# Performance work log

Measured on AMD Instinct MI355X. Metric: run time of the kernel, lower is better.

## Reference

```python
import jax, jax.numpy as jnp
import numpy as np

N, E, F, EF, H = 10000, 320000, 512, 6, 256


def _lin(k, fan_in, fan_out):
    # torch.nn.Linear default init
    s = 1.0 / np.sqrt(fan_in)
    kw, kb = jax.random.split(k)
    W = jax.random.uniform(kw, (fan_in, fan_out), minval=-s, maxval=s, dtype=jnp.float32)
    b = jax.random.uniform(kb, (fan_out,), minval=-s, maxval=s, dtype=jnp.float32)
    return W, b


def setup_inputs() -> dict:
    key = jax.random.key(0)
    ks = jax.random.split(key, 13)
    inp = {}
    inp["x"] = jax.random.normal(ks[0], (N, F), dtype=jnp.float32)
    inp["edge_index"] = jax.random.randint(ks[1], (2, E), 0, N, dtype=jnp.int32)
    inp["edge_attr"] = jax.random.normal(ks[2], (E, EF), dtype=jnp.float32)
    shapes = {
        "We0a": (2 * F + EF, H), "We0b": (H, H),   # conv_in edge MLP
        "Wn0a": (F + H, H),      "Wn0b": (H, H),   # conv_in node MLP
        "We1a": (3 * H, H),      "We1b": (H, H),   # conv[0] edge MLP
        "Wn1a": (2 * H, H),      "Wn1b": (H, H),   # conv[0] node MLP
        "Wp1":  (H, H),          "Wp2":  (H, 1),   # EdgePredictorFromEdges
    }
    for i, (nm, (fi, fo)) in enumerate(shapes.items()):
        W, b = _lin(ks[3 + i % 10], fi, fo)
        inp[nm] = W
        inp["b" + nm[1:]] = b
    return inp


def _mp(x, src, dst, ea, Wea, bea, Web, beb, Wna, bna, Wnb, bnb, residual, agg_mean):
    # MetaLayer edge model: MLP(concat[x_i, x_j, edge_attr])
    e_in = jnp.concatenate([x[src], x[dst], ea], axis=-1)   # [E, ...]
    new_ea = jax.nn.relu(e_in @ Wea + bea) @ Web + beb
    if residual:
        new_ea = new_ea + ea
    # node model: aggregate incoming edges at dst, MLP(concat[x, agg])
    agg = jax.ops.segment_sum(new_ea, dst, num_segments=N)  # [N, H]
    if agg_mean:
        deg = jax.ops.segment_sum(jnp.ones((src.shape[0],), x.dtype), dst, num_segments=N)
        agg = agg / jnp.maximum(deg, 1.0)[:, None]
    n_in = jnp.concatenate([x, agg], axis=-1)
    new_x = jax.nn.relu(n_in @ Wna + bna) @ Wnb + bnb
    if residual:
        new_x = new_x + x
    return new_x, new_ea


def reference(x, edge_index, edge_attr,
              We0a, be0a, We0b, be0b, Wn0a, bn0a, Wn0b, bn0b,
              We1a, be1a, We1b, be1b, Wn1a, bn1a, Wn1b, bn1b,
              Wp1, bp1, Wp2, bp2):
    src, dst = edge_index[0], edge_index[1]
    # conv_in: dims change (F->H, EF->H) so no residual; base_aggregation='mean'
    x1, ea1 = _mp(x, src, dst, edge_attr, We0a, be0a, We0b, be0b,
                  Wn0a, bn0a, Wn0b, bn0b, residual=False, agg_mean=True)
    # conv[0]: dims match -> residual; default base_aggregation='sum'
    x2, ea2 = _mp(x1, src, dst, ea1, We1a, be1a, We1b, be1b,
                  Wn1a, bn1a, Wn1b, bn1b, residual=True, agg_mean=False)
    # EdgePredictorFromEdges (eval mode -> dropout is identity)
    h = jax.nn.leaky_relu(ea2 @ Wp1 + bp1)
    out = (h @ Wp2 + bp2)[:, 0]  # squeeze -> [E]
    return out
```

## Files before the change

### kernel.cpp

```cpp
#include <hip/hip_runtime.h>

#define N_NODES 10000
#define N_EDGES 320000
#define HD      256

typedef __attribute__((ext_vector_type(8))) short bf16x8;
typedef __attribute__((ext_vector_type(4))) float f32x4;
#define MFMA16 __builtin_amdgcn_mfma_f32_16x16x32_bf16

#define OFF_PD   2560000
#define OFF_BA   5120000
#define OFF_BB   7680000
#define OFF_BC   10240000
#define OFF_DEG  12800000
#define OFF_BCV  12810000
#define OFF_BAV  12810256
#define OFF_PW0  12810512

__device__ __forceinline__ ushort f2bf(float x) {
  union { float f; unsigned u; } c; c.f = x;
  unsigned r = (c.u + 0x7FFFu + ((c.u >> 16) & 1u)) >> 16;
  return (ushort)r;
}
__device__ __forceinline__ float bf2f(ushort h) {
  union { float f; unsigned u; } c; c.u = ((unsigned)h) << 16; return c.f;
}

__global__ __launch_bounds__(256)
void prep_split(const float* __restrict__ W, ushort* __restrict__ H,
                ushort* __restrict__ L)
{
  int slot = blockIdx.x * 256 + threadIdx.x;
  int s    = slot >> 10;
  int rem  = slot & 1023;
  int cf   = rem >> 6;
  int lane = rem & 63;
  int k0 = s * 32 + ((lane >> 4) << 3);
  int n  = cf * 16 + (lane & 15);
#pragma unroll
  for (int j = 0; j < 8; ++j) {
    float v = W[(k0 + j) * HD + n];
    ushort hi = f2bf(v);
    H[slot * 8 + j] = hi;
    L[slot * 8 + j] = f2bf(v - bf2f(hi));
  }
}

__global__ __launch_bounds__(256)
void node_gemm(const float* __restrict__ A1, int K1,
               const float* __restrict__ A2, int K2,
               const float* __restrict__ scale,
               const float* __restrict__ W,
               const float* __restrict__ bias,
               float* __restrict__ C, int M, int act)
{
  __shared__ float sA[64 * 36];
  __shared__ float sB[32 * 256];
  __shared__ float sBias[256];
  const int tid = threadIdx.x;
  const int r0  = blockIdx.x * 64;
  if (bias) sBias[tid] = bias[tid];
  const int ty = tid >> 4, tx = tid & 15;

  float acc[4][16];
#pragma unroll
  for (int r = 0; r < 4; r++)
#pragma unroll
    for (int c = 0; c < 16; c++) acc[r][c] = 0.f;

  const int K = K1 + K2;
  const int arow = tid >> 2;
  const int aks  = (tid & 3) * 8;
  const int gr_a = r0 + arow;

  for (int kb = 0; kb < K; kb += 32) {
    const float* Ap; int lda, koff; float sc = 1.0f;
    if (kb < K1) { Ap = A1; lda = K1; koff = kb; }
    else { Ap = A2; lda = K2; koff = kb - K1;
           if (scale) sc = scale[gr_a < M ? gr_a : M - 1]; }
#pragma unroll
    for (int j = 0; j < 8; j += 4) {
      float4 v;
      if (gr_a < M) v = *(const float4*)&Ap[(long)gr_a * lda + koff + aks + j];
      else { v.x = v.y = v.z = v.w = 0.f; }
      v.x *= sc; v.y *= sc; v.z *= sc; v.w *= sc;
      *(float4*)&sA[arow * 36 + aks + j] = v;
    }
#pragma unroll
    for (int j = 0; j < 8; j++) {
      int i = tid + 256 * j, row = i >> 6, c4 = i & 63;
      *(float4*)&sB[row * HD + c4 * 4] = *(const float4*)&W[(long)(kb + row) * HD + c4 * 4];
    }
    __syncthreads();
#pragma unroll 4
    for (int kk = 0; kk < 32; kk++) {
      float a0 = sA[(ty * 4 + 0) * 36 + kk];
      float a1 = sA[(ty * 4 + 1) * 36 + kk];
      float a2 = sA[(ty * 4 + 2) * 36 + kk];
      float a3 = sA[(ty * 4 + 3) * 36 + kk];
#pragma unroll
      for (int c = 0; c < 16; c++) {
        float b = sB[kk * HD + tx + 16 * c];
        acc[0][c] += a0 * b; acc[1][c] += a1 * b;
        acc[2][c] += a2 * b; acc[3][c] += a3 * b;
      }
    }
    __syncthreads();
  }

#pragma unroll
  for (int r = 0; r < 4; r++) {
    int gr = r0 + ty * 4 + r;
    if (gr >= M) continue;
#pragma unroll
    for (int c = 0; c < 16; c++) {
      int col = tx + 16 * c;
      float v = acc[r][c];
      if (bias) v += sBias[col];
      if (act)  v = fmaxf(v, 0.f);
      C[(long)gr * HD + col] = v;
    }
  }
}

__global__ __launch_bounds__(256)
void bias_fold_k(const float* __restrict__ v1, const float* __restrict__ v2,
                 const float* __restrict__ W, const float* __restrict__ base,
                 float* __restrict__ out)
{
  const int j = threadIdx.x;
  float s = base[j];
  for (int k = 0; k < HD; k++) {
    float v = v1[k] + (v2 ? v2[k] : 0.f);
    s += v * W[k * HD + j];
  }
  out[j] = s;
}

__global__ void rdeg_k(float* __restrict__ deg)
{
  int i = blockIdx.x * blockDim.x + threadIdx.x;
  if (i < N_NODES) deg[i] = 1.0f / fmaxf(deg[i], 1.0f);
}

__device__ __forceinline__ void build_h0(
    int tid, const float* __restrict__ Ps, const float* __restrict__ Pd,
    const float* __restrict__ eattr, long e0,
    const float* __restrict__ W6, const float* __restrict__ b0,
    const int* sSrc, const int* sDst, ushort* Ah, ushort* Al)
{
  const int el = tid >> 3, q = tid & 7;
  const int sv = sSrc[el], dv = sDst[el];
  const long e = e0 + el;
  float eav[6];
#pragma unroll
  for (int k = 0; k < 6; ++k) eav[k] = eattr[e * 6 + k];
  const float* ps = Ps + (long)sv * HD + q * 32;
  const float* pd = Pd + (long)dv * HD + q * 32;
  const int sw = (el & 7) << 4;
  char* ahB = (char*)Ah + el * 512;
  char* alB = (char*)Al + el * 512;
#pragma unroll
  for (int jj = 0; jj < 8; ++jj) {
    float4 a  = *(const float4*)(ps + jj * 4);
    float4 b  = *(const float4*)(pd + jj * 4);
    float4 bb = *(const float4*)(b0 + q * 32 + jj * 4);
    float vx = a.x + b.x + bb.x;
    float vy = a.y + b.y + bb.y;
    float vz = a.z + b.z + bb.z;
    float vw = a.w + b.w + bb.w;
#pragma unroll
    for (int k = 0; k < 6; ++k) {
      float4 w = *(const float4*)(W6 + k * HD + q * 32 + jj * 4);
      vx += eav[k] * w.x; vy += eav[k] * w.y;
      vz += eav[k] * w.z; vw += eav[k] * w.w;
    }
    vx = fmaxf(vx, 0.f); vy = fmaxf(vy, 0.f);
    vz = fmaxf(vz, 0.f); vw = fmaxf(vw, 0.f);
    ushort4 hh, ll;
    hh.x = f2bf(vx); hh.y = f2bf(vy); hh.z = f2bf(vz); hh.w = f2bf(vw);
    ll.x = f2bf(vx - bf2f(hh.x)); ll.y = f2bf(vy - bf2f(hh.y));
    ll.z = f2bf(vz - bf2f(hh.z)); ll.w = f2bf(vw - bf2f(hh.w));
    const int off = (q * 64 + jj * 8) ^ sw;
    *(ushort4*)(ahB + off) = hh;
    *(ushort4*)(alB + off) = ll;
  }
}

__device__ __forceinline__ void write_split(ushort* Ah, ushort* Al,
                                            int row, int col, float v)
{
  const int off = row * 512 + ((col * 2) ^ ((row & 7) << 4));
  ushort hi = f2bf(v);
  *(ushort*)((char*)Ah + off) = hi;
  *(ushort*)((char*)Al + off) = f2bf(v - bf2f(hi));
}

__device__ __forceinline__ void load_afrag(const ushort* Ah, const ushort* Al,
    int row, int s, int lane, bf16x8& ah, bf16x8& al)
{
  const int aoff = row * 512 + ((((s << 6) + ((lane >> 4) << 4))) ^ ((row & 7) << 4));
  ah = *(const bf16x8*)((const char*)Ah + aoff);
  al = *(const bf16x8*)((const char*)Al + aoff);
}

__device__ __forceinline__ void gemm_pass(
    const ushort* __restrict__ pW,
    const ushort* Ah, const ushort* Al,
    int lane, int wc, int wrg, f32x4 acc[2][4])
{
  const bf16x8* pH = (const bf16x8*)pW;
  const bf16x8* pL = (const bf16x8*)(pW + 65536);
#pragma unroll 2
  for (int s = 0; s < 8; ++s) {
    bf16x8 ah[2], al[2];
#pragma unroll
    for (int rb = 0; rb < 2; ++rb)
      load_afrag(Ah, Al, (wrg * 2 + rb) * 16 + (lane & 15), s, lane, ah[rb], al[rb]);
#pragma unroll
    for (int cf = 0; cf < 4; ++cf) {
      const int slot = s * 1024 + (wc * 4 + cf) * 64 + lane;
      bf16x8 bh = pH[slot];
      bf16x8 bl = pL[slot];
#pragma unroll
      for (int rb = 0; rb < 2; ++rb) {
        acc[rb][cf] = MFMA16(al[rb], bh, acc[rb][cf], 0, 0, 0);
        acc[rb][cf] = MFMA16(ah[rb], bl, acc[rb][cf], 0, 0, 0);
        acc[rb][cf] = MFMA16(ah[rb], bh, acc[rb][cf], 0, 0, 0);
      }
    }
  }
}

__global__ __launch_bounds__(512, 4)
void edge_conv_in(const int* __restrict__ ei, const float* __restrict__ eattr,
                  const float* __restrict__ Ps, const float* __restrict__ Pd,
                  const float* __restrict__ W6, const float* __restrict__ b0,
                  const ushort* __restrict__ pW0,
                  const float* __restrict__ be0b,
                  float* __restrict__ agg, float* __restrict__ deg)
{
  __shared__ ushort Ah[64 * 256];
  __shared__ ushort Al[64 * 256];
  __shared__ int    sSrc[64], sDst[64];
  const int tid = threadIdx.x;
  const long e0 = (long)blockIdx.x * 64;

  if (tid < 64) {
    int dv = ei[N_EDGES + e0 + tid];
    sDst[tid] = dv;
    atomicAdd(&deg[dv], 1.0f);
  } else if (tid < 128) {
    sSrc[tid - 64] = ei[e0 + tid - 64];
  }
  __syncthreads();

  build_h0(tid, Ps, Pd, eattr, e0, W6, b0, sSrc, sDst, Ah, Al);
  __syncthreads();

  const int lane = tid & 63, wid = tid >> 6;
  const int wc = wid & 3, wrg = wid >> 2;

  f32x4 acc[2][4];
#pragma unroll
  for (int rb = 0; rb < 2; ++rb)
#pragma unroll
    for (int cf = 0; cf < 4; ++cf) acc[rb][cf] = (f32x4){0.f, 0.f, 0.f, 0.f};
  gemm_pass(pW0, Ah, Al, lane, wc, wrg, acc);

#pragma unroll
  for (int rb = 0; rb < 2; ++rb) {
    const int rbase = (wrg * 2 + rb) * 16 + ((lane >> 4) << 2);
#pragma unroll
    for (int cf = 0; cf < 4; ++cf) {
      const int col = wc * 64 + cf * 16 + (lane & 15);
      const float bv = be0b[col];
#pragma unroll
      for (int r = 0; r < 4; ++r)
        atomicAdd(&agg[(long)sDst[rbase + r] * HD + col], acc[rb][cf][r] + bv);
    }
  }
}

__global__ __launch_bounds__(512, 4)
void edge_pred(const int* __restrict__ ei, const float* __restrict__ eattr,
               const float* __restrict__ Ps, const float* __restrict__ Pd,
               const float* __restrict__ W6, const float* __restrict__ b0,
               const float* __restrict__ P1s, const float* __restrict__ P1d,
               const ushort* __restrict__ pWA, const ushort* __restrict__ pWB,
               const ushort* __restrict__ pWc,
               const float* __restrict__ bA, const float* __restrict__ bc,
               const float* __restrict__ Wp2, const float* __restrict__ bp2,
               float* __restrict__ out)
{
  __shared__ ushort Ah[64 * 256];
  __shared__ ushort Al[64 * 256];
  __shared__ float  sOut[64];
  __shared__ int    sSrc[64], sDst[64];
  const int tid = threadIdx.x;
  const long e0 = (long)blockIdx.x * 64;

  if (tid < 64) {
    sDst[tid] = ei[N_EDGES + e0 + tid];
    sOut[tid] = bp2[0];
  } else if (tid < 128) {
    sSrc[tid - 64] = ei[e0 + tid - 64];
  }
  __syncthreads();

  build_h0(tid, Ps, Pd, eattr, e0, W6, b0, sSrc, sDst, Ah, Al);
  __syncthreads();

  const int lane = tid & 63, wid = tid >> 6;
  const int wc = wid & 3, wrg = wid >> 2;

  f32x4 acc1[2][4];
#pragma unroll
  for (int rb = 0; rb < 2; ++rb)
#pragma unroll
    for (int cf = 0; cf < 4; ++cf) acc1[rb][cf] = (f32x4){0.f, 0.f, 0.f, 0.f};
  gemm_pass(pWA, Ah, Al, lane, wc, wrg, acc1);

  f32x4 accT[2][4];
#pragma unroll
  for (int rb = 0; rb < 2; ++rb)
#pragma unroll
    for (int cf = 0; cf < 4; ++cf) accT[rb][cf] = (f32x4){0.f, 0.f, 0.f, 0.f};
  gemm_pass(pWB, Ah, Al, lane, wc, wrg, accT);
  __syncthreads();

#pragma unroll
  for (int rb = 0; rb < 2; ++rb) {
    const int rbase = (wrg * 2 + rb) * 16 + ((lane >> 4) << 2);
#pragma unroll
    for (int cf = 0; cf < 4; ++cf) {
      const int col = wc * 64 + cf * 16 + (lane & 15);
      const float bv = bA[col];
#pragma unroll
      for (int r = 0; r < 4; ++r) {
        const int row = rbase + r;
        float v = acc1[rb][cf][r] + P1s[(long)sSrc[row] * HD + col]
                                  + P1d[(long)sDst[row] * HD + col] + bv;
        write_split(Ah, Al, row, col, fmaxf(v, 0.f));
      }
    }
  }
  __syncthreads();

  f32x4 accZ[2][4];
#pragma unroll
  for (int rb = 0; rb < 2; ++rb)
#pragma unroll
    for (int cf = 0; cf < 4; ++cf) accZ[rb][cf] = (f32x4){0.f, 0.f, 0.f, 0.f};
  gemm_pass(pWc, Ah, Al, lane, wc, wrg, accZ);

  float p[2][4] = {{0.f,0.f,0.f,0.f},{0.f,0.f,0.f,0.f}};
#pragma unroll
  for (int cf = 0; cf < 4; ++cf) {
    const int col = wc * 64 + cf * 16 + (lane & 15);
    const float w   = Wp2[col];
    const float bcv = bc[col];
#pragma unroll
    for (int rb = 0; rb < 2; ++rb)
#pragma unroll
      for (int r = 0; r < 4; ++r) {
        float z = accZ[rb][cf][r] + accT[rb][cf][r] + bcv;
        z = z > 0.f ? z : 0.01f * z;
        p[rb][r] += z * w;
      }
  }
#pragma unroll
  for (int rb = 0; rb < 2; ++rb)
#pragma unroll
    for (int r = 0; r < 4; ++r) {
      p[rb][r] += __shfl_xor(p[rb][r], 1);
      p[rb][r] += __shfl_xor(p[rb][r], 2);
      p[rb][r] += __shfl_xor(p[rb][r], 4);
      p[rb][r] += __shfl_xor(p[rb][r], 8);
    }
  if ((lane & 15) == 0) {
#pragma unroll
    for (int rb = 0; rb < 2; ++rb) {
      const int rbase = (wrg * 2 + rb) * 16 + ((lane >> 4) << 2);
#pragma unroll
      for (int r = 0; r < 4; ++r) atomicAdd(&sOut[rbase + r], p[rb][r]);
    }
  }
  __syncthreads();
  if (tid < 64) out[e0 + tid] = sOut[tid];
}

extern "C" void kernel_launch(void* const* d_in, const int* in_sizes, int n_in,
                              void* d_out, int out_size, void* d_ws, size_t ws_size,
                              hipStream_t stream)
{
  const float* x     = (const float*)d_in[0];
  const int*   ei    = (const int*)d_in[1];
  const float* eattr = (const float*)d_in[2];
  const float* We0a  = (const float*)d_in[3];
  const float* be0a  = (const float*)d_in[4];
  const float* We0b  = (const float*)d_in[5];
  const float* be0b  = (const float*)d_in[6];
  const float* Wn0a  = (const float*)d_in[7];
  const float* bn0a  = (const float*)d_in[8];
  const float* Wn0b  = (const float*)d_in[9];
  const float* bn0b  = (const float*)d_in[10];
  const float* We1a  = (const float*)d_in[11];
  const float* be1a  = (const float*)d_in[12];
  const float* We1b  = (const float*)d_in[13];
  const float* be1b  = (const float*)d_in[14];
  const float* Wp1   = (const float*)d_in[19];
  const float* bp1   = (const float*)d_in[20];
  const float* Wp2   = (const float*)d_in[21];
  const float* bp2   = (const float*)d_in[22];
  float* out = (float*)d_out;
  float* ws  = (float*)d_ws;

  float* P_s  = ws;
  float* P_d  = ws + OFF_PD;
  float* bufA = ws + OFF_BA;
  float* bufB = ws + OFF_BB;
  float* bufC = ws + OFF_BC;
  float* deg  = ws + OFF_DEG;
  float* bcB  = ws + OFF_BCV;
  float* bAB  = ws + OFF_BAV;
  ushort* pW0 = (ushort*)(ws + OFF_PW0);

  float*  WAf = ws + OFF_BB;
  float*  WBf = ws + OFF_BB + 65536;
  float*  WcF = ws + OFF_BB + 131072;
  ushort* pWA = (ushort*)(ws + OFF_BB + 196608);
  ushort* pWB = (ushort*)(ws + OFF_BB + 262144);
  ushort* pWc = (ushort*)(ws + OFF_BB + 327680);

  const float* W6  = We0a + 1024 * HD;
  const float* WeE = We1a + 512 * HD;

  hipMemsetAsync(bufC, 0, (2560000 + 10000) * sizeof(float), stream);

  const int ngrid = (N_NODES + 63) / 64;
  const int egrid = N_EDGES / 64;

  node_gemm<<<ngrid, 256, 0, stream>>>(x, 512, nullptr, 0, nullptr, We0a,            nullptr, P_s, N_NODES, 0);
  node_gemm<<<ngrid, 256, 0, stream>>>(x, 512, nullptr, 0, nullptr, We0a + 512 * HD, nullptr, P_d, N_NODES, 0);
  prep_split<<<32, 256, 0, stream>>>(We0b, pW0, pW0 + 65536);
  bias_fold_k<<<1, 256, 0, stream>>>(be1b, be0b, Wp1, bp1, bcB);
  bias_fold_k<<<1, 256, 0, stream>>>(be0b, nullptr, WeE, be1a, bAB);

  edge_conv_in<<<egrid, 512, 0, stream>>>(ei, eattr, P_s, P_d, W6, be0a,
                                          pW0, be0b, bufC, deg);
  rdeg_k<<<(N_NODES + 255) / 256, 256, 0, stream>>>(deg);

  node_gemm<<<ngrid, 256, 0, stream>>>(x, 512, bufC, 256, deg, Wn0a, bn0a, bufA, N_NODES, 1);
  node_gemm<<<ngrid, 256, 0, stream>>>(bufA, 256, nullptr, 0, nullptr, Wn0b, bn0b, bufB, N_NODES, 0);
  node_gemm<<<ngrid, 256, 0, stream>>>(bufB, 256, nullptr, 0, nullptr, We1a,            nullptr, bufA, N_NODES, 0);
  node_gemm<<<ngrid, 256, 0, stream>>>(bufB, 256, nullptr, 0, nullptr, We1a + 256 * HD, nullptr, bufC, N_NODES, 0);

  node_gemm<<<4, 256, 0, stream>>>(We0b, 256, nullptr, 0, nullptr, WeE, nullptr, WAf, 256, 0);
  node_gemm<<<4, 256, 0, stream>>>(We0b, 256, nullptr, 0, nullptr, Wp1, nullptr, WBf, 256, 0);
  node_gemm<<<4, 256, 0, stream>>>(We1b, 256, nullptr, 0, nullptr, Wp1, nullptr, WcF, 256, 0);
  prep_split<<<32, 256, 0, stream>>>(WAf, pWA, pWA + 65536);
  prep_split<<<32, 256, 0, stream>>>(WBf, pWB, pWB + 65536);
  prep_split<<<32, 256, 0, stream>>>(WcF, pWc, pWc + 65536);

  edge_pred<<<egrid, 512, 0, stream>>>(ei, eattr, P_s, P_d, W6, be0a,
      bufA, bufC, pWA, pWB, pWc, bAB, bcB, Wp2, bp2, out);
}
```

Baseline: 2.453 ms.

## Retile edge GEMM waves to full-row column strips with B-fragment prefetch

Changes the per-wave MFMA tile from 32 rows x 64 columns to 64 rows x 32 columns, so each wave loads half as many weight fragments from global memory but reads all A fragments from LDS. Adds register double-buffering that prefetches the next k-step's weight fragments while the current step's MFMAs run, and fully unrolls the k loop. This aims to cut global/L2 weight traffic and hide its latency, at the cost of more LDS reads and higher register pressure under the existing launch bounds.

```diff
diff --git a/kernel.cpp b/kernel.cpp
--- a/kernel.cpp
+++ b/kernel.cpp
@@ -207,27 +207,43 @@
 __device__ __forceinline__ void gemm_pass(
     const ushort* __restrict__ pW,
     const ushort* Ah, const ushort* Al,
-    int lane, int wc, int wrg, f32x4 acc[2][4])
+    int lane, int wid, f32x4 acc[4][2])
 {
   const bf16x8* pH = (const bf16x8*)pW;
   const bf16x8* pL = (const bf16x8*)(pW + 65536);
-#pragma unroll 2
+  const int cbase = wid * 2 * 64 + lane;
+  bf16x8 bh[2], bl[2];
+#pragma unroll
+  for (int cf = 0; cf < 2; ++cf) {
+    bh[cf] = pH[cbase + cf * 64];
+    bl[cf] = pL[cbase + cf * 64];
+  }
+#pragma unroll
   for (int s = 0; s < 8; ++s) {
-    bf16x8 ah[2], al[2];
-#pragma unroll
-    for (int rb = 0; rb < 2; ++rb)
-      load_afrag(Ah, Al, (wrg * 2 + rb) * 16 + (lane & 15), s, lane, ah[rb], al[rb]);
-#pragma unroll
-    for (int cf = 0; cf < 4; ++cf) {
-      const int slot = s * 1024 + (wc * 4 + cf) * 64 + lane;
-      bf16x8 bh = pH[slot];
-      bf16x8 bl = pL[slot];
-#pragma unroll
-      for (int rb = 0; rb < 2; ++rb) {
-        acc[rb][cf] = MFMA16(al[rb], bh, acc[rb][cf], 0, 0, 0);
-        acc[rb][cf] = MFMA16(ah[rb], bl, acc[rb][cf], 0, 0, 0);
-        acc[rb][cf] = MFMA16(ah[rb], bh, acc[rb][cf], 0, 0, 0);
+    bf16x8 nbh[2], nbl[2];
+    if (s < 7) {
+      const int slotn = (s + 1) * 1024 + cbase;
+#pragma unroll
+      for (int cf = 0; cf < 2; ++cf) {
+        nbh[cf] = pH[slotn + cf * 64];
+        nbl[cf] = pL[slotn + cf * 64];
       }
+    }
+    bf16x8 ah[4], al[4];
+#pragma unroll
+    for (int rb = 0; rb < 4; ++rb)
+      load_afrag(Ah, Al, rb * 16 + (lane & 15), s, lane, ah[rb], al[rb]);
+#pragma unroll
+    for (int cf = 0; cf < 2; ++cf)
+#pragma unroll
+      for (int rb = 0; rb < 4; ++rb) {
+        acc[rb][cf] = MFMA16(al[rb], bh[cf], acc[rb][cf], 0, 0, 0);
+        acc[rb][cf] = MFMA16(ah[rb], bl[cf], acc[rb][cf], 0, 0, 0);
+        acc[rb][cf] = MFMA16(ah[rb], bh[cf], acc[rb][cf], 0, 0, 0);
+      }
+    if (s < 7) {
+#pragma unroll
+      for (int cf = 0; cf < 2; ++cf) { bh[cf] = nbh[cf]; bl[cf] = nbl[cf]; }
     }
   }
 }
@@ -259,21 +275,20 @@
   __syncthreads();
 
   const int lane = tid & 63, wid = tid >> 6;
-  const int wc = wid & 3, wrg = wid >> 2;
-
-  f32x4 acc[2][4];
-#pragma unroll
-  for (int rb = 0; rb < 2; ++rb)
-#pragma unroll
-    for (int cf = 0; cf < 4; ++cf) acc[rb][cf] = (f32x4){0.f, 0.f, 0.f, 0.f};
-  gemm_pass(pW0, Ah, Al, lane, wc, wrg, acc);
-
-#pragma unroll
-  for (int rb = 0; rb < 2; ++rb) {
-    const int rbase = (wrg * 2 + rb) * 16 + ((lane >> 4) << 2);
-#pragma unroll
-    for (int cf = 0; cf < 4; ++cf) {
-      const int col = wc * 64 + cf * 16 + (lane & 15);
+
+  f32x4 acc[4][2];
+#pragma unroll
+  for (int rb = 0; rb < 4; ++rb)
+#pragma unroll
+    for (int cf = 0; cf < 2; ++cf) acc[rb][cf] = (f32x4){0.f, 0.f, 0.f, 0.f};
+  gemm_pass(pW0, Ah, Al, lane, wid, acc);
+
+#pragma unroll
+  for (int rb = 0; rb < 4; ++rb) {
+    const int rbase = rb * 16 + ((lane >> 4) << 2);
+#pragma unroll
+    for (int cf = 0; cf < 2; ++cf) {
+      const int col = wid * 32 + cf * 16 + (lane & 15);
       const float bv = be0b[col];
 #pragma unroll
       for (int r = 0; r < 4; ++r)
@@ -312,29 +327,28 @@
   __syncthreads();
 
   const int lane = tid & 63, wid = tid >> 6;
-  const int wc = wid & 3, wrg = wid >> 2;
-
-  f32x4 acc1[2][4];
-#pragma unroll
-  for (int rb = 0; rb < 2; ++rb)
-#pragma unroll
-    for (int cf = 0; cf < 4; ++cf) acc1[rb][cf] = (f32x4){0.f, 0.f, 0.f, 0.f};
-  gemm_pass(pWA, Ah, Al, lane, wc, wrg, acc1);
-
-  f32x4 accT[2][4];
-#pragma unroll
-  for (int rb = 0; rb < 2; ++rb)
-#pragma unroll
-    for (int cf = 0; cf < 4; ++cf) accT[rb][cf] = (f32x4){0.f, 0.f, 0.f, 0.f};
-  gemm_pass(pWB, Ah, Al, lane, wc, wrg, accT);
-  __syncthreads();
-
-#pragma unroll
-  for (int rb = 0; rb < 2; ++rb) {
-    const int rbase = (wrg * 2 + rb) * 16 + ((lane >> 4) << 2);
-#pragma unroll
-    for (int cf = 0; cf < 4; ++cf) {
-      const int col = wc * 64 + cf * 16 + (lane & 15);
+
+  f32x4 acc1[4][2];
+#pragma unroll
+  for (int rb = 0; rb < 4; ++rb)
+#pragma unroll
+    for (int cf = 0; cf < 2; ++cf) acc1[rb][cf] = (f32x4){0.f, 0.f, 0.f, 0.f};
+  gemm_pass(pWA, Ah, Al, lane, wid, acc1);
+
+  f32x4 accT[4][2];
+#pragma unroll
+  for (int rb = 0; rb < 4; ++rb)
+#pragma unroll
+    for (int cf = 0; cf < 2; ++cf) accT[rb][cf] = (f32x4){0.f, 0.f, 0.f, 0.f};
+  gemm_pass(pWB, Ah, Al, lane, wid, accT);
+  __syncthreads();
+
+#pragma unroll
+  for (int rb = 0; rb < 4; ++rb) {
+    const int rbase = rb * 16 + ((lane >> 4) << 2);
+#pragma unroll
+    for (int cf = 0; cf < 2; ++cf) {
+      const int col = wid * 32 + cf * 16 + (lane & 15);
       const float bv = bA[col];
 #pragma unroll
       for (int r = 0; r < 4; ++r) {
@@ -347,21 +361,25 @@
   }
   __syncthreads();
 
-  f32x4 accZ[2][4];
-#pragma unroll
-  for (int rb = 0; rb < 2; ++rb)
-#pragma unroll
-    for (int cf = 0; cf < 4; ++cf) accZ[rb][cf] = (f32x4){0.f, 0.f, 0.f, 0.f};
-  gemm_pass(pWc, Ah, Al, lane, wc, wrg, accZ);
-
-  float p[2][4] = {{0.f,0.f,0.f,0.f},{0.f,0.f,0.f,0.f}};
-#pragma unroll
-  for (int cf = 0; cf < 4; ++cf) {
-    const int col = wc * 64 + cf * 16 + (lane & 15);
+  f32x4 accZ[4][2];
+#pragma unroll
+  for (int rb = 0; rb < 4; ++rb)
+#pragma unroll
+    for (int cf = 0; cf < 2; ++cf) accZ[rb][cf] = (f32x4){0.f, 0.f, 0.f, 0.f};
+  gemm_pass(pWc, Ah, Al, lane, wid, accZ);
+
+  float p[4][4];
+#pragma unroll
+  for (int rb = 0; rb < 4; ++rb)
+#pragma unroll
+    for (int r = 0; r < 4; ++r) p[rb][r] = 0.f;
+#pragma unroll
+  for (int cf = 0; cf < 2; ++cf) {
+    const int col = wid * 32 + cf * 16 + (lane & 15);
     const float w   = Wp2[col];
     const float bcv = bc[col];
 #pragma unroll
-    for (int rb = 0; rb < 2; ++rb)
+    for (int rb = 0; rb < 4; ++rb)
 #pragma unroll
       for (int r = 0; r < 4; ++r) {
         float z = accZ[rb][cf][r] + accT[rb][cf][r] + bcv;
@@ -370,7 +388,7 @@
       }
   }
 #pragma unroll
-  for (int rb = 0; rb < 2; ++rb)
+  for (int rb = 0; rb < 4; ++rb)
 #pragma unroll
     for (int r = 0; r < 4; ++r) {
       p[rb][r] += __shfl_xor(p[rb][r], 1);
@@ -380,8 +398,8 @@
     }
   if ((lane & 15) == 0) {
 #pragma unroll
-    for (int rb = 0; rb < 2; ++rb) {
-      const int rbase = (wrg * 2 + rb) * 16 + ((lane >> 4) << 2);
+    for (int rb = 0; rb < 4; ++rb) {
+      const int rbase = rb * 16 + ((lane >> 4) << 2);
 #pragma unroll
       for (int r = 0; r < 4; ++r) atomicAdd(&sOut[rbase + r], p[rb][r]);
     }
```

Result: faster. 2.387 ms (-2.7%).
